# Performance work log

Measured on AMD Instinct MI355X. Metric: run time of the kernel, lower is better.

The kernel has to match this reference:

```python
import jax, jax.numpy as jnp
import numpy as np
from jax.scipy.linalg import solve_triangular

H, VD, M = 16, 64, 128
RIDGE = 0.01


def setup_inputs() -> dict:
    key = jax.random.key(0)
    ks = jax.random.split(key, 9)
    B, L, HD = 4, 2048, 1024
    s = 1.0 / np.sqrt(HD).astype(np.float32)
    return {
        "x": jax.random.normal(ks[0], (B, L, HD), dtype=jnp.float32),
        "cur_k": jnp.zeros((1,), dtype=jnp.float32),
        "input_mask": jnp.ones((B, L), dtype=jnp.float32),
        "Wq": jax.random.normal(ks[1], (HD, HD), dtype=jnp.float32) * s,
        "Wk": jax.random.normal(ks[2], (HD, HD), dtype=jnp.float32) * s,
        "Wv": jax.random.normal(ks[3], (HD, HD), dtype=jnp.float32) * s,
        "Wo": jax.random.normal(ks[4], (HD, HD), dtype=jnp.float32) * s,
        "bo": jax.random.normal(ks[5], (HD,), dtype=jnp.float32) * s,
        "rff_W": jax.random.normal(ks[6], (H, VD, M), dtype=jnp.float32),  # / lengthscale=1.0
        "rff_b": 2.0 * np.pi * jax.random.uniform(ks[7], (H, M), dtype=jnp.float32),
    }


def reference(x, cur_k, input_mask, Wq, Wk, Wv, Wo, bo, rff_W, rff_b):
    B, L, HD = x.shape
    scale = jnp.asarray(1.0 / np.sqrt(M), dtype=x.dtype)
    M2 = 2 * M

    def heads(t):  # [B,L,HD] -> [B,H,L,VD]
        return t.reshape(B, L, H, VD).transpose(0, 2, 1, 3)

    q = heads(x @ Wq.T)
    k = heads(x @ Wk.T)
    v = heads(x @ Wv.T)

    mask = input_mask[:, :L].astype(x.dtype)
    qmask = mask[:, None, :, None]  # [B,1,L,1]

    def rff(X):  # [B,H,L,VD] -> [B,H,L,2M]
        proj = jnp.einsum('bhld,hdm->bhlm', X, rff_W) + rff_b[None, :, None, :]
        return scale * jnp.concatenate([jnp.cos(proj), jnp.sin(proj)], axis=-1)

    PhiQ = rff(q)
    PhiK_w = rff(k) * qmask
    V_w = v * qmask

    G = jnp.einsum('bhlm,bhln->bhmn', PhiK_w, PhiK_w)  # [B,H,2M,2M]
    G = G + RIDGE * jnp.eye(M2, dtype=x.dtype)
    T = jnp.einsum('bhlm,bhld->bhmd', PhiK_w, V_w)      # [B,H,2M,VD]

    Lch = jnp.linalg.cholesky(G)
    y = solve_triangular(Lch, T, lower=True)
    W = solve_triangular(jnp.swapaxes(Lch, -2, -1), y, lower=False)

    out = jnp.einsum('bhlm,bhmd->bhld', PhiQ, W)        # [B,H,L,VD]
    # unsqueeze sample dim, permute to [B,1,L,H,VD], flatten heads -> [B,1,L,HD]
    samples = jnp.transpose(out, (0, 2, 1, 3)).reshape(B, L, HD)[:, None]
    samples = samples @ Wo.T + bo                        # W_O (dropout: eval no-op)
    samples = samples * qmask                            # [B,1,L,1] broadcast
    return samples
```

## Files before the change

kernel.cpp:

```cpp
#include <hip/hip_runtime.h>
#include <math.h>

#define B_ 4
#define L_ 2048
#define HD_ 1024
#define H_ 16
#define VD_ 64
#define M_ 128
#define M2_ 256
#define RIDGE_ 0.01f
#define SCALE_ 0.08838834764831845f

typedef unsigned short u16;
typedef __attribute__((ext_vector_type(8))) short short8;
typedef __attribute__((ext_vector_type(4))) float floatx4;

__device__ __forceinline__ u16 f2bf(float x) {
  unsigned u = __float_as_uint(x);
  unsigned r = u + 0x7fff + ((u >> 16) & 1);
  return (u16)(r >> 16);
}
__device__ __forceinline__ float bf2f(u16 h) {
  return __uint_as_float(((unsigned)h) << 16);
}
__device__ __forceinline__ void gload_lds16(const u16* g, u16* l) {
  __builtin_amdgcn_global_load_lds(
      (const __attribute__((address_space(1))) unsigned int*)g,
      (__attribute__((address_space(3))) unsigned int*)l, 16, 0, 0);
}
__device__ __forceinline__ void split4(float4 f, ushort4* h, float4* r) {
  h->x = f2bf(f.x); h->y = f2bf(f.y); h->z = f2bf(f.z); h->w = f2bf(f.w);
  r->x = f.x - bf2f(h->x); r->y = f.y - bf2f(h->y);
  r->z = f.z - bf2f(h->z); r->w = f.w - bf2f(h->w);
}

__global__ __launch_bounds__(256) void cvt_split_kernel(
    const float* __restrict__ src, u16* __restrict__ hi, u16* __restrict__ lo, int n4)
{
  int i = blockIdx.x * 256 + threadIdx.x;
  if (i < n4) {
    float4 f = ((const float4*)src)[i];
    ushort4 hv; float4 r;
    split4(f, &hv, &r);
    ushort4 lv = {f2bf(r.x), f2bf(r.y), f2bf(r.z), f2bf(r.w)};
    ((ushort4*)hi)[i] = hv;
    ((ushort4*)lo)[i] = lv;
  }
}

__global__ __launch_bounds__(256) void mfma_nt(
    const u16* __restrict__ A0, const u16* __restrict__ B0,
    float* __restrict__ C, int Ndim, int Kdim, int ldA, int ldB,
    const float* __restrict__ bias, const float* __restrict__ mask)
{
  __shared__ __align__(16) u16 a_sm[4096];
  __shared__ __align__(16) u16 b_sm[4096];
  const int tid = threadIdx.x;
  const int wave = tid >> 6, lane = tid & 63;
  const int m0 = blockIdx.y * 128, n0 = blockIdx.x * 128;
  const int wrow = (wave >> 1) * 64, wcol = (wave & 1) * 64;
  const int fm = lane & 15, q = lane >> 4;

  floatx4 acc[4][4];
#pragma unroll
  for (int i = 0; i < 4; ++i)
#pragma unroll
    for (int j = 0; j < 4; ++j) acc[i][j] = (floatx4){0.f, 0.f, 0.f, 0.f};

  const u16* Ag0 = A0 + (long)(m0 + lane) * ldA + wave * 8;
  const u16* Ag1 = A0 + (long)(m0 + 64 + lane) * ldA + wave * 8;
  const u16* Bg0 = B0 + (long)(n0 + lane) * ldB + wave * 8;
  const u16* Bg1 = B0 + (long)(n0 + 64 + lane) * ldB + wave * 8;
  u16* la0 = &a_sm[(wave * 128 + 0) * 8];
  u16* la1 = &a_sm[(wave * 128 + 64) * 8];
  u16* lb0 = &b_sm[(wave * 128 + 0) * 8];
  u16* lb1 = &b_sm[(wave * 128 + 64) * 8];

  for (int k0 = 0; k0 < Kdim; k0 += 32) {
    __syncthreads();
    gload_lds16(Ag0 + k0, la0);
    gload_lds16(Ag1 + k0, la1);
    gload_lds16(Bg0 + k0, lb0);
    gload_lds16(Bg1 + k0, lb1);
    __syncthreads();
    short8 af[4], bf[4];
#pragma unroll
    for (int i = 0; i < 4; ++i)
      af[i] = *(const short8*)&a_sm[(q * 128 + wrow + i * 16 + fm) * 8];
#pragma unroll
    for (int j = 0; j < 4; ++j)
      bf[j] = *(const short8*)&b_sm[(q * 128 + wcol + j * 16 + fm) * 8];
#pragma unroll
    for (int i = 0; i < 4; ++i)
#pragma unroll
      for (int j = 0; j < 4; ++j)
        acc[i][j] = __builtin_amdgcn_mfma_f32_16x16x32_bf16(af[i], bf[j], acc[i][j], 0, 0, 0);
  }

  const int colb = n0 + wcol + fm;
  const int rbase = m0 + wrow + (lane >> 4) * 4;
#pragma unroll
  for (int j = 0; j < 4; ++j) {
    int cg = colb + j * 16;
    float bb = bias ? bias[cg] : 0.f;
#pragma unroll
    for (int i = 0; i < 4; ++i) {
#pragma unroll
      for (int r = 0; r < 4; ++r) {
        int row = rbase + i * 16 + r;
        float val = acc[i][j][r];
        if (bias) val = (val + bb) * mask[row];
        C[(long)row * Ndim + cg] = val;
      }
    }
  }
}

__global__ __launch_bounds__(256) void mfma_qk3(
    const u16* __restrict__ Ah, const u16* __restrict__ Al,
    const u16* __restrict__ Bh, const u16* __restrict__ Bl,
    float* __restrict__ Cq, float* __restrict__ Ck)
{
  __shared__ __align__(16) u16 ah_sm[4096], al_sm[4096];
  __shared__ __align__(16) u16 bh_sm[4096], bl_sm[4096];
  const int tid = threadIdx.x;
  const int wave = tid >> 6, lane = tid & 63;
  const int m0 = blockIdx.y * 128, n0 = blockIdx.x * 128;
  const int wrow = (wave >> 1) * 64, wcol = (wave & 1) * 64;
  const int fm = lane & 15, q = lane >> 4;

  floatx4 acc[4][4];
#pragma unroll
  for (int i = 0; i < 4; ++i)
#pragma unroll
    for (int j = 0; j < 4; ++j) acc[i][j] = (floatx4){0.f, 0.f, 0.f, 0.f};

  const long a0o = (long)(m0 + lane) * 1024 + wave * 8;
  const long a1o = (long)(m0 + 64 + lane) * 1024 + wave * 8;
  const long b0o = (long)(n0 + lane) * 1024 + wave * 8;
  const long b1o = (long)(n0 + 64 + lane) * 1024 + wave * 8;
  u16* lah0 = &ah_sm[(wave * 128 + 0) * 8];
  u16* lah1 = &ah_sm[(wave * 128 + 64) * 8];
  u16* lal0 = &al_sm[(wave * 128 + 0) * 8];
  u16* lal1 = &al_sm[(wave * 128 + 64) * 8];
  u16* lbh0 = &bh_sm[(wave * 128 + 0) * 8];
  u16* lbh1 = &bh_sm[(wave * 128 + 64) * 8];
  u16* lbl0 = &bl_sm[(wave * 128 + 0) * 8];
  u16* lbl1 = &bl_sm[(wave * 128 + 64) * 8];

  for (int k0 = 0; k0 < 1024; k0 += 32) {
    __syncthreads();
    gload_lds16(Ah + a0o + k0, lah0);
    gload_lds16(Ah + a1o + k0, lah1);
    gload_lds16(Al + a0o + k0, lal0);
    gload_lds16(Al + a1o + k0, lal1);
    gload_lds16(Bh + b0o + k0, lbh0);
    gload_lds16(Bh + b1o + k0, lbh1);
    gload_lds16(Bl + b0o + k0, lbl0);
    gload_lds16(Bl + b1o + k0, lbl1);
    __syncthreads();
    short8 afh[4], afl[4], bfh[4], bfl[4];
#pragma unroll
    for (int i = 0; i < 4; ++i) {
      afh[i] = *(const short8*)&ah_sm[(q * 128 + wrow + i * 16 + fm) * 8];
      afl[i] = *(const short8*)&al_sm[(q * 128 + wrow + i * 16 + fm) * 8];
    }
#pragma unroll
    for (int j = 0; j < 4; ++j) {
      bfh[j] = *(const short8*)&bh_sm[(q * 128 + wcol + j * 16 + fm) * 8];
      bfl[j] = *(const short8*)&bl_sm[(q * 128 + wcol + j * 16 + fm) * 8];
    }
#pragma unroll
    for (int i = 0; i < 4; ++i)
#pragma unroll
      for (int j = 0; j < 4; ++j) {
        acc[i][j] = __builtin_amdgcn_mfma_f32_16x16x32_bf16(afh[i], bfh[j], acc[i][j], 0, 0, 0);
        acc[i][j] = __builtin_amdgcn_mfma_f32_16x16x32_bf16(afl[i], bfh[j], acc[i][j], 0, 0, 0);
        acc[i][j] = __builtin_amdgcn_mfma_f32_16x16x32_bf16(afh[i], bfl[j], acc[i][j], 0, 0, 0);
      }
  }

  float* Cp; int cb;
  if (n0 < 1024) { Cp = Cq; cb = n0; }
  else           { Cp = Ck; cb = n0 - 1024; }
  const int colb = cb + wcol + fm;
  const int rbase = m0 + wrow + (lane >> 4) * 4;
#pragma unroll
  for (int j = 0; j < 4; ++j) {
    int cg = colb + j * 16;
#pragma unroll
    for (int i = 0; i < 4; ++i)
#pragma unroll
      for (int r = 0; r < 4; ++r)
        Cp[(long)(rbase + i * 16 + r) * 1024 + cg] = acc[i][j][r];
  }
}

__global__ __launch_bounds__(256) void rff_k_t(
    const float* __restrict__ src, const float* __restrict__ mask,
    const float* __restrict__ rffW, const float* __restrict__ rffb,
    u16* __restrict__ pkh, u16* __restrict__ pkl, int b0)
{
  __shared__ __align__(16) float w_lds[64][132];
  __shared__ __align__(16) float x_lds[64][68];
  __shared__ float b_lds[128];
  const int l0 = blockIdx.x * 64;
  const int h = blockIdx.y, b = b0 + blockIdx.z;
  const int zloc = blockIdx.z * 16 + h;
  const int tid = threadIdx.x;

  const float* wsrc = rffW + h * 8192;
  for (int f = tid * 4; f < 8192; f += 1024) {
    int d = f >> 7, m = f & 127;
    *(float4*)&w_lds[d][m] = *(const float4*)&wsrc[f];
  }
  if (tid < 128) b_lds[tid] = rffb[h * 128 + tid];
  {
    int r = tid >> 2, c0 = (tid & 3) * 16;
    const float* srow = src + (long)(b * L_ + l0 + r) * 1024 + h * VD_ + c0;
    *(float4*)&x_lds[r][c0 + 0]  = *(const float4*)(srow + 0);
    *(float4*)&x_lds[r][c0 + 4]  = *(const float4*)(srow + 4);
    *(float4*)&x_lds[r][c0 + 8]  = *(const float4*)(srow + 8);
    *(float4*)&x_lds[r][c0 + 12] = *(const float4*)(srow + 12);
  }
  __syncthreads();

  const int ty = tid >> 4, tx = tid & 15;
  float acc[4][8];
  {
    float4 bb0 = *(const float4*)&b_lds[4 * tx];
    float4 bb1 = *(const float4*)&b_lds[4 * tx + 64];
#pragma unroll
    for (int i = 0; i < 4; ++i) {
      acc[i][0] = bb0.x; acc[i][1] = bb0.y; acc[i][2] = bb0.z; acc[i][3] = bb0.w;
      acc[i][4] = bb1.x; acc[i][5] = bb1.y; acc[i][6] = bb1.z; acc[i][7] = bb1.w;
    }
  }
#pragma unroll 8
  for (int kk = 0; kk < 64; ++kk) {
    float4 w0 = *(const float4*)&w_lds[kk][4 * tx];
    float4 w1 = *(const float4*)&w_lds[kk][4 * tx + 64];
    float xv[4];
#pragma unroll
    for (int i = 0; i < 4; ++i) xv[i] = x_lds[4 * ty + i][kk];
#pragma unroll
    for (int i = 0; i < 4; ++i) {
      acc[i][0] = fmaf(xv[i], w0.x, acc[i][0]);
      acc[i][1] = fmaf(xv[i], w0.y, acc[i][1]);
      acc[i][2] = fmaf(xv[i], w0.z, acc[i][2]);
      acc[i][3] = fmaf(xv[i], w0.w, acc[i][3]);
      acc[i][4] = fmaf(xv[i], w1.x, acc[i][4]);
      acc[i][5] = fmaf(xv[i], w1.y, acc[i][5]);
      acc[i][6] = fmaf(xv[i], w1.z, acc[i][6]);
      acc[i][7] = fmaf(xv[i], w1.w, acc[i][7]);
    }
  }
  float fi[4];
#pragma unroll
  for (int i = 0; i < 4; ++i) fi[i] = SCALE_ * mask[b * L_ + l0 + 4 * ty + i];
  float cvv[4][8], svv[4][8];
#pragma unroll
  for (int i = 0; i < 4; ++i)
#pragma unroll
    for (int jj = 0; jj < 8; ++jj) {
      float sv, cv;
      sincosf(acc[i][jj], &sv, &cv);
      cvv[i][jj] = cv * fi[i];
      svv[i][jj] = sv * fi[i];
    }
  const long lbase = l0 + 4 * ty;
  const long zbase = (long)zloc * 655360;
#pragma unroll
  for (int jj = 0; jj < 8; ++jj) {
    int mcol = (jj < 4) ? (4 * tx + jj) : (64 + 4 * tx + (jj - 4));
    ushort4 h4, l4;
    h4.x = f2bf(cvv[0][jj]); l4.x = f2bf(cvv[0][jj] - bf2f(h4.x));
    h4.y = f2bf(cvv[1][jj]); l4.y = f2bf(cvv[1][jj] - bf2f(h4.y));
    h4.z = f2bf(cvv[2][jj]); l4.z = f2bf(cvv[2][jj] - bf2f(h4.z));
    h4.w = f2bf(cvv[3][jj]); l4.w = f2bf(cvv[3][jj] - bf2f(h4.w));
    long base = zbase + (long)mcol * 2048 + lbase;
    *(ushort4*)&pkh[base] = h4;
    *(ushort4*)&pkl[base] = l4;
    ushort4 hs, ls;
    hs.x = f2bf(svv[0][jj]); ls.x = f2bf(svv[0][jj] - bf2f(hs.x));
    hs.y = f2bf(svv[1][jj]); ls.y = f2bf(svv[1][jj] - bf2f(hs.y));
    hs.z = f2bf(svv[2][jj]); ls.z = f2bf(svv[2][jj] - bf2f(hs.z));
    hs.w = f2bf(svv[3][jj]); ls.w = f2bf(svv[3][jj] - bf2f(hs.w));
    long base2 = zbase + (long)(mcol + 128) * 2048 + lbase;
    *(ushort4*)&pkh[base2] = hs;
    *(ushort4*)&pkl[base2] = ls;
  }
}

__global__ __launch_bounds__(256) void vt_kernel(
    const float* __restrict__ v, const float* __restrict__ mask,
    u16* __restrict__ pkh, u16* __restrict__ pkl, int b0)
{
  __shared__ float t[128][65];
  const int z = blockIdx.y;
  const int b = b0 + (z >> 4), h = z & 15;
  const int l0 = blockIdx.x * 128;
  const int tid = threadIdx.x;
  const int d = tid & 63, lg = tid >> 6;
  for (int i = 0; i < 128; i += 4) {
    int ll = i + lg;
    float mv = mask[b * L_ + l0 + ll];
    t[ll][d] = v[(long)(b * L_ + l0 + ll) * 1024 + h * 64 + d] * mv;
  }
  __syncthreads();
  const int d2 = tid >> 2, lofs = (tid & 3) * 32;
  long base = (long)z * 655360 + (long)(256 + d2) * 2048 + l0 + lofs;
  for (int j = 0; j < 32; j += 4) {
    float f0 = t[lofs + j + 0][d2], f1 = t[lofs + j + 1][d2];
    float f2 = t[lofs + j + 2][d2], f3 = t[lofs + j + 3][d2];
    ushort4 hv, lv;
    hv.x = f2bf(f0); lv.x = f2bf(f0 - bf2f(hv.x));
    hv.y = f2bf(f1); lv.y = f2bf(f1 - bf2f(hv.y));
    hv.z = f2bf(f2); lv.z = f2bf(f2 - bf2f(hv.z));
    hv.w = f2bf(f3); lv.w = f2bf(f3 - bf2f(hv.w));
    *(ushort4*)&pkh[base + j] = hv;
    *(ushort4*)&pkl[base + j] = lv;
  }
}

__global__ __launch_bounds__(256) void mfma_gt(
    const u16* __restrict__ pkh, const u16* __restrict__ pkl,
    float* __restrict__ Gp, float* __restrict__ Tp, int bh0)
{
  __shared__ __align__(16) u16 ah_sm[4096], al_sm[4096];
  __shared__ __align__(16) u16 bh_sm[2048], bl_sm[2048];
  const int tid = threadIdx.x;
  const int wave = tid >> 6, lane = tid & 63;
  const int z = blockIdx.z;
  const int mt = blockIdx.y & 1, kc = blockIdx.y >> 1;
  const int m0 = mt * 128, n0 = blockIdx.x * 64;
  const int wrow = (wave >> 1) * 64, wcol = (wave & 1) * 32;
  const int fm = lane & 15, q = lane >> 4;
  const long batch = (long)z * 655360;
  const u16* Ah = pkh + batch;
  const u16* Al = pkl + batch;

  floatx4 acc[4][2];
#pragma unroll
  for (int i = 0; i < 4; ++i)
#pragma unroll
    for (int j = 0; j < 2; ++j) acc[i][j] = (floatx4){0.f, 0.f, 0.f, 0.f};

  const long a0o = (long)(m0 + lane) * 2048 + wave * 8;
  const long a1o = (long)(m0 + 64 + lane) * 2048 + wave * 8;
  const long b0o = (long)(n0 + lane) * 2048 + wave * 8;
  u16* lah0 = &ah_sm[(wave * 128 + 0) * 8];
  u16* lah1 = &ah_sm[(wave * 128 + 64) * 8];
  u16* lal0 = &al_sm[(wave * 128 + 0) * 8];
  u16* lal1 = &al_sm[(wave * 128 + 64) * 8];
  u16* lbh = &bh_sm[(wave * 64) * 8];
  u16* lbl = &bl_sm[(wave * 64) * 8];

  const int kbeg = kc * 1024, kend = kbeg + 1024;
  for (int k0 = kbeg; k0 < kend; k0 += 32) {
    __syncthreads();
    gload_lds16(Ah + a0o + k0, lah0);
    gload_lds16(Ah + a1o + k0, lah1);
    gload_lds16(Al + a0o + k0, lal0);
    gload_lds16(Al + a1o + k0, lal1);
    gload_lds16(Ah + b0o + k0, lbh);
    gload_lds16(Al + b0o + k0, lbl);
    __syncthreads();
    short8 afh[4], afl[4], bfh[2], bfl[2];
#pragma unroll
    for (int i = 0; i < 4; ++i) {
      afh[i] = *(const short8*)&ah_sm[(q * 128 + wrow + i * 16 + fm) * 8];
      afl[i] = *(const short8*)&al_sm[(q * 128 + wrow + i * 16 + fm) * 8];
    }
#pragma unroll
    for (int j = 0; j < 2; ++j) {
      bfh[j] = *(const short8*)&bh_sm[(q * 64 + wcol + j * 16 + fm) * 8];
      bfl[j] = *(const short8*)&bl_sm[(q * 64 + wcol + j * 16 + fm) * 8];
    }
#pragma unroll
    for (int i = 0; i < 4; ++i)
#pragma unroll
      for (int j = 0; j < 2; ++j) {
        acc[i][j] = __builtin_amdgcn_mfma_f32_16x16x32_bf16(afh[i], bfh[j], acc[i][j], 0, 0, 0);
        acc[i][j] = __builtin_amdgcn_mfma_f32_16x16x32_bf16(afl[i], bfh[j], acc[i][j], 0, 0, 0);
        acc[i][j] = __builtin_amdgcn_mfma_f32_16x16x32_bf16(afh[i], bfl[j], acc[i][j], 0, 0, 0);
      }
  }

  const int bh = bh0 + z;
  float* Gb = Gp + (long)kc * 4194304;
  float* Tb = Tp + (long)kc * 1048576;
  const int rbase = m0 + wrow + (lane >> 4) * 4;
#pragma unroll
  for (int j = 0; j < 2; ++j) {
    int col = n0 + wcol + j * 16 + fm;
#pragma unroll
    for (int i = 0; i < 4; ++i)
#pragma unroll
      for (int r = 0; r < 4; ++r) {
        int row = rbase + i * 16 + r;
        float val = acc[i][j][r];
        if (n0 < 256) Gb[(long)bh * 65536 + (long)row * 256 + col] = val;
        else Tb[(long)bh * 16384 + (long)row * 64 + (col - 256)] = val;
      }
  }
}

__global__ __launch_bounds__(256) void reduce_gt_kernel(
    const float* __restrict__ Gp, float* __restrict__ G,
    const float* __restrict__ Tp, float* __restrict__ T)
{
  long i = (long)blockIdx.x * 256 + threadIdx.x;
  if (i < 1048576) {
    float4 a = ((const float4*)Gp)[i];
    float4 b = ((const float4*)(Gp + 4194304))[i];
    float4 o = {a.x + b.x, a.y + b.y, a.z + b.z, a.w + b.w};
    ((float4*)G)[i] = o;
  } else {
    long j = i - 1048576;
    float4 a = ((const float4*)Tp)[j];
    float4 b = ((const float4*)(Tp + 1048576))[j];
    float4 o = {a.x + b.x, a.y + b.y, a.z + b.z, a.w + b.w};
    ((float4*)T)[j] = o;
  }
}

__global__ __launch_bounds__(256) void mfma_out_k(
    const u16* __restrict__ ph, const u16* __restrict__ pl,
    const u16* __restrict__ wth, const u16* __restrict__ wtl,
    u16* __restrict__ oh)
{
  __shared__ __align__(16) u16 ah_sm[4096], al_sm[4096];
  __shared__ __align__(16) u16 bh_sm[2048], bl_sm[2048];
  const int tid = threadIdx.x;
  const int wave = tid >> 6, lane = tid & 63;
  const int bh = blockIdx.y;
  const int b = bh >> 4, h = bh & 15;
  const int l0 = blockIdx.x * 128;
  const int wrow = (wave >> 1) * 64, wcol = (wave & 1) * 32;
  const int fm = lane & 15, q = lane >> 4;
  const u16* Ah = ph + (long)bh * 524288 + (long)l0 * 256;
  const u16* Al = pl + (long)bh * 524288 + (long)l0 * 256;
  const u16* Bh = wth + (long)bh * 16384;
  const u16* Bl = wtl + (long)bh * 16384;

  floatx4 acc[4][2];
#pragma unroll
  for (int i = 0; i < 4; ++i)
#pragma unroll
    for (int j = 0; j < 2; ++j) acc[i][j] = (floatx4){0.f, 0.f, 0.f, 0.f};

  const long a0o = (long)lane * 256 + wave * 8;
  const long a1o = (long)(64 + lane) * 256 + wave * 8;
  const long b0o = (long)lane * 256 + wave * 8;
  u16* lah0 = &ah_sm[(wave * 128 + 0) * 8];
  u16* lah1 = &ah_sm[(wave * 128 + 64) * 8];
  u16* lal0 = &al_sm[(wave * 128 + 0) * 8];
  u16* lal1 = &al_sm[(wave * 128 + 64) * 8];
  u16* lbh = &bh_sm[(wave * 64) * 8];
  u16* lbl = &bl_sm[(wave * 64) * 8];

  for (int k0 = 0; k0 < 256; k0 += 32) {
    __syncthreads();
    gload_lds16(Ah + a0o + k0, lah0);
    gload_lds16(Ah + a1o + k0, lah1);
    gload_lds16(Al + a0o + k0, lal0);
    gload_lds16(Al + a1o + k0, lal1);
    gload_lds16(Bh + b0o + k0, lbh);
    gload_lds16(Bl + b0o + k0, lbl);
    __syncthreads();
    short8 afh[4], afl[4], bfh[2], bfl[2];
#pragma unroll
    for (int i = 0; i < 4; ++i) {
      afh[i] = *(const short8*)&ah_sm[(q * 128 + wrow + i * 16 + fm) * 8];
      afl[i] = *(const short8*)&al_sm[(q * 128 + wrow + i * 16 + fm) * 8];
    }
#pragma unroll
    for (int j = 0; j < 2; ++j) {
      bfh[j] = *(const short8*)&bh_sm[(q * 64 + wcol + j * 16 + fm) * 8];
      bfl[j] = *(const short8*)&bl_sm[(q * 64 + wcol + j * 16 + fm) * 8];
    }
#pragma unroll
    for (int i = 0; i < 4; ++i)
#pragma unroll
      for (int j = 0; j < 2; ++j) {
        acc[i][j] = __builtin_amdgcn_mfma_f32_16x16x32_bf16(afh[i], bfh[j], acc[i][j], 0, 0, 0);
        acc[i][j] = __builtin_amdgcn_mfma_f32_16x16x32_bf16(afl[i], bfh[j], acc[i][j], 0, 0, 0);
        acc[i][j] = __builtin_amdgcn_mfma_f32_16x16x32_bf16(afh[i], bfl[j], acc[i][j], 0, 0, 0);
      }
  }

  const int rbase = l0 + wrow + (lane >> 4) * 4;
#pragma unroll
  for (int j = 0; j < 2; ++j) {
    int col = h * 64 + wcol + j * 16 + fm;
#pragma unroll
    for (int i = 0; i < 4; ++i)
#pragma unroll
      for (int r = 0; r < 4; ++r)
        oh[(long)(b * L_ + rbase + i * 16 + r) * 1024 + col] = f2bf(acc[i][j][r]);
  }
}

__global__ __launch_bounds__(512) void chol_rffq_wo_kernel(
    float* __restrict__ Gw,
    const float* __restrict__ qsrc,
    const float* __restrict__ rffW, const float* __restrict__ rffb,
    u16* __restrict__ ph, u16* __restrict__ pl,
    const float* __restrict__ Wo, u16* __restrict__ wo_hi)
{
  extern __shared__ float sm[];
  const int bx = blockIdx.x;
  const int tid = threadIdx.x;

  if (bx < 64) {
    float* panel = sm;
    float* invD  = sm + 4352;
    float* Gb = Gw + (long)bx * 65536;

    for (int p = 0; p < 16; ++p) {
      if (tid < 64) {
        const int i = tid & 15;
        float r[16];
#pragma unroll
        for (int k = 0; k < 16; ++k) r[k] = Gb[(16 * p + i) * 256 + 16 * p + k];
        r[i] += RIDGE_;
#pragma unroll
        for (int j = 0; j < 16; ++j) {
          float dj = __shfl(r[j], j);
          float dinv = 1.0f / sqrtf(dj);
          r[j] *= dinv;
          float Lij = r[j];
#pragma unroll
          for (int k = j + 1; k < 16; ++k) {
            float Lkj = __shfl(r[j], k);
            r[k] = fmaf(-Lij, Lkj, r[k]);
          }
        }
        float x[16];
#pragma unroll
        for (int j = 0; j < 16; ++j) {
          float s = (i == j) ? 1.0f : 0.0f;
#pragma unroll
          for (int k = 0; k < j; ++k) {
            float Ljk = __shfl(r[k], j);
            s = fmaf(-Ljk, x[k], s);
          }
          float Ljj = __shfl(r[j], j);
          x[j] = s / Ljj;
        }
        if (tid < 16) {
#pragma unroll
          for (int j = 0; j < 16; ++j) {
            invD[j * 17 + tid] = x[j];
            Gb[(16 * p + j) * 256 + 16 * p + tid] = x[j];
          }
        }
      }
      __syncthreads();

      const int nIb = 15 - p;
      if (nIb == 0) break;
      const int nrows = nIb * 16;
      const int r0 = 16 * (p + 1);

      for (int f = tid; f < nrows * 16; f += 512) {
        int rr = f >> 4, cc = f & 15;
        panel[(r0 + rr) * 17 + cc] = Gb[(long)(r0 + rr) * 256 + 16 * p + cc];
      }
      __syncthreads();

      float outv[8];
#pragma unroll
      for (int s = 0; s < 8; ++s) {
        int f = tid + s * 512;
        if (f < nrows * 16) {
          int rr = f >> 4, j = f & 15;
          const float* arow = &panel[(r0 + rr) * 17];
          const float* dcol = &invD[j * 17];
          float s2 = 0.f;
#pragma unroll
          for (int k = 0; k < 16; ++k) s2 = fmaf(arow[k], dcol[k], s2);
          outv[s] = s2;
        }
      }
      __syncthreads();
#pragma unroll
      for (int s = 0; s < 8; ++s) {
        int f = tid + s * 512;
        if (f < nrows * 16) {
          int rr = f >> 4, j = f & 15;
          panel[(r0 + rr) * 17 + j] = outv[s];
          Gb[(long)(r0 + rr) * 256 + 16 * p + j] = outv[s];
        }
      }
      __syncthreads();

      const int npairs = nIb * (nIb + 1) / 2;
      const int g = tid >> 4, t = tid & 15;
      const int tx = t & 3, ty = t >> 2;
      for (int pi0 = 0; pi0 < npairs; pi0 += 32) {
        int pi = pi0 + g;
        if (pi < npairs) {
          int a = 0; while ((a + 1) * (a + 2) / 2 <= pi) ++a;
          int b2 = pi - a * (a + 1) / 2;
          int I = p + 1 + a, J = p + 1 + b2;
          float c4[4][4];
#pragma unroll
          for (int ii = 0; ii < 4; ++ii) {
            float4 cv = *(const float4*)&Gb[(long)(16 * I + 4 * ty + ii) * 256 + 16 * J + 4 * tx];
            c4[ii][0] = cv.x; c4[ii][1] = cv.y; c4[ii][2] = cv.z; c4[ii][3] = cv.w;
          }
#pragma unroll
          for (int kk = 0; kk < 16; ++kk) {
            float av[4], bv[4];
#pragma unroll
            for (int ii = 0; ii < 4; ++ii) av[ii] = panel[(16 * I + 4 * ty + ii) * 17 + kk];
#pragma unroll
            for (int jj = 0; jj < 4; ++jj) bv[jj] = panel[(16 * J + 4 * tx + jj) * 17 + kk];
#pragma unroll
            for (int ii = 0; ii < 4; ++ii)
#pragma unroll
              for (int jj = 0; jj < 4; ++jj)
                c4[ii][jj] = fmaf(-av[ii], bv[jj], c4[ii][jj]);
          }
#pragma unroll
          for (int ii = 0; ii < 4; ++ii) {
            float4 cv = {c4[ii][0], c4[ii][1], c4[ii][2], c4[ii][3]};
            *(float4*)&Gb[(long)(16 * I + 4 * ty + ii) * 256 + 16 * J + 4 * tx] = cv;
          }
        }
      }
      __syncthreads();
    }
  } else if (bx < 64 + 2048) {
    const int id = bx - 64;
    const int l0 = (id & 31) * 64;
    const int h = (id >> 5) & 15;
    const int b = id >> 9;
    float* w_lds = sm;
    float* x_lds = sm + 8448;
    float* b_lds = sm + 12800;

    const float* wsrc = rffW + h * 8192;
    for (int f = tid * 4; f < 8192; f += 2048) {
      int d = f >> 7, m = f & 127;
      *(float4*)&w_lds[d * 132 + m] = *(const float4*)&wsrc[f];
    }
    if (tid < 128) b_lds[tid] = rffb[h * 128 + tid];
    {
      int r = tid >> 3, c0 = (tid & 7) * 8;
      const float* srow = qsrc + (long)(b * L_ + l0 + r) * 1024 + h * VD_ + c0;
      *(float4*)&x_lds[r * 68 + c0 + 0] = *(const float4*)(srow + 0);
      *(float4*)&x_lds[r * 68 + c0 + 4] = *(const float4*)(srow + 4);
    }
    __syncthreads();

    const int sub = tid >> 8;
    const int t = tid & 255;
    const int ty = t >> 4, tx = t & 15;
    const int rrow = sub * 32 + 2 * ty;
    float acc[2][8];
    {
      float4 bb0 = *(const float4*)&b_lds[4 * tx];
      float4 bb1 = *(const float4*)&b_lds[4 * tx + 64];
#pragma unroll
      for (int i = 0; i < 2; ++i) {
        acc[i][0] = bb0.x; acc[i][1] = bb0.y; acc[i][2] = bb0.z; acc[i][3] = bb0.w;
        acc[i][4] = bb1.x; acc[i][5] = bb1.y; acc[i][6] = bb1.z; acc[i][7] = bb1.w;
      }
    }
#pragma unroll 8
    for (int kk = 0; kk < 64; ++kk) {
      float4 w0 = *(const float4*)&w_lds[kk * 132 + 4 * tx];
      float4 w1 = *(const float4*)&w_lds[kk * 132 + 4 * tx + 64];
      float xv[2];
#pragma unroll
      for (int i = 0; i < 2; ++i) xv[i] = x_lds[(rrow + i) * 68 + kk];
#pragma unroll
      for (int i = 0; i < 2; ++i) {
        acc[i][0] = fmaf(xv[i], w0.x, acc[i][0]);
        acc[i][1] = fmaf(xv[i], w0.y, acc[i][1]);
        acc[i][2] = fmaf(xv[i], w0.z, acc[i][2]);
        acc[i][3] = fmaf(xv[i], w0.w, acc[i][3]);
        acc[i][4] = fmaf(xv[i], w1.x, acc[i][4]);
        acc[i][5] = fmaf(xv[i], w1.y, acc[i][5]);
        acc[i][6] = fmaf(xv[i], w1.z, acc[i][6]);
        acc[i][7] = fmaf(xv[i], w1.w, acc[i][7]);
      }
    }
#pragma unroll
    for (int i = 0; i < 2; ++i) {
      int l = l0 + rrow + i;
      float4 c0, c1, s0, s1;
      float sv, cv;
      sincosf(acc[i][0], &sv, &cv); c0.x = cv * SCALE_; s0.x = sv * SCALE_;
      sincosf(acc[i][1], &sv, &cv); c0.y = cv * SCALE_; s0.y = sv * SCALE_;
      sincosf(acc[i][2], &sv, &cv); c0.z = cv * SCALE_; s0.z = sv * SCALE_;
      sincosf(acc[i][3], &sv, &cv); c0.w = cv * SCALE_; s0.w = sv * SCALE_;
      sincosf(acc[i][4], &sv, &cv); c1.x = cv * SCALE_; s1.x = sv * SCALE_;
      sincosf(acc[i][5], &sv, &cv); c1.y = cv * SCALE_; s1.y = sv * SCALE_;
      sincosf(acc[i][6], &sv, &cv); c1.z = cv * SCALE_; s1.z = sv * SCALE_;
      sincosf(acc[i][7], &sv, &cv); c1.w = cv * SCALE_; s1.w = sv * SCALE_;
      long base = ((long)(b * H_ + h) * L_ + l) * M2_;
      ushort4 hv; float4 r4;
      split4(c0, &hv, &r4);
      *(ushort4*)&ph[base + 4 * tx] = hv;
      *(ushort4*)&pl[base + 4 * tx] = (ushort4){f2bf(r4.x), f2bf(r4.y), f2bf(r4.z), f2bf(r4.w)};
      split4(c1, &hv, &r4);
      *(ushort4*)&ph[base + 64 + 4 * tx] = hv;
      *(ushort4*)&pl[base + 64 + 4 * tx] = (ushort4){f2bf(r4.x), f2bf(r4.y), f2bf(r4.z), f2bf(r4.w)};
      split4(s0, &hv, &r4);
      *(ushort4*)&ph[base + 128 + 4 * tx] = hv;
      *(ushort4*)&pl[base + 128 + 4 * tx] = (ushort4){f2bf(r4.x), f2bf(r4.y), f2bf(r4.z), f2bf(r4.w)};
      split4(s1, &hv, &r4);
      *(ushort4*)&ph[base + 192 + 4 * tx] = hv;
      *(ushort4*)&pl[base + 192 + 4 * tx] = (ushort4){f2bf(r4.x), f2bf(r4.y), f2bf(r4.z), f2bf(r4.w)};
    }
  } else {
    const int id2 = bx - (64 + 2048);
    int idx = id2 * 512 + tid;
    for (int i = idx; i < 262144; i += 65536) {
      float4 f = ((const float4*)Wo)[i];
      ushort4 hv = {f2bf(f.x), f2bf(f.y), f2bf(f.z), f2bf(f.w)};
      ((ushort4*)wo_hi)[i] = hv;
    }
  }
}

__global__ __launch_bounds__(256) void tri_solve_kernel(
    const float* __restrict__ Gw, const float* __restrict__ T,
    u16* __restrict__ wth, u16* __restrict__ wtl)
{
  __shared__ float Y[256 * 17];
  __shared__ float tmp[16 * 17];
  const int bh = blockIdx.y;
  const int d0 = blockIdx.x * 16;
  const int tid = threadIdx.x;
  const int i = tid >> 4, d = tid & 15;
  const float* Gb = Gw + (long)bh * 65536;
  const float* Tb = T + (long)bh * 16384;

  for (int r = i; r < 256; r += 16) Y[r * 17 + d] = Tb[r * 64 + d0 + d];
  __syncthreads();

  for (int J = 0; J < 16; ++J) {
    float acc = Y[(J * 16 + i) * 17 + d];
    for (int c = 0; c < J; ++c) {
      const float* Lblk = &Gb[(long)(16 * J + i) * 256 + 16 * c];
#pragma unroll
      for (int k = 0; k < 16; k += 4) {
        float4 l4 = *(const float4*)&Lblk[k];
        acc = fmaf(-l4.x, Y[(c * 16 + k + 0) * 17 + d], acc);
        acc = fmaf(-l4.y, Y[(c * 16 + k + 1) * 17 + d], acc);
        acc = fmaf(-l4.z, Y[(c * 16 + k + 2) * 17 + d], acc);
        acc = fmaf(-l4.w, Y[(c * 16 + k + 3) * 17 + d], acc);
      }
    }
    tmp[i * 17 + d] = acc;
    __syncthreads();
    const float* invD = &Gb[(long)(16 * J + i) * 256 + 16 * J];
    float y = 0.f;
#pragma unroll
    for (int k = 0; k < 16; ++k) y = fmaf(invD[k], tmp[k * 17 + d], y);
    Y[(J * 16 + i) * 17 + d] = y;
    __syncthreads();
  }

  for (int J = 15; J >= 0; --J) {
    float acc = Y[(J * 16 + i) * 17 + d];
    for (int I = J + 1; I < 16; ++I) {
#pragma unroll
      for (int k = 0; k < 16; ++k)
        acc = fmaf(-Gb[(long)(16 * I + k) * 256 + 16 * J + i], Y[(I * 16 + k) * 17 + d], acc);
    }
    tmp[i * 17 + d] = acc;
    __syncthreads();
    float w = 0.f;
#pragma unroll
    for (int k = 0; k < 16; ++k)
      w = fmaf(Gb[(long)(16 * J + k) * 256 + 16 * J + i], tmp[k * 17 + d], w);
    Y[(J * 16 + i) * 17 + d] = w;
    __syncthreads();
  }

  for (int f = tid; f < 16 * 256; f += 256) {
    int dc = f >> 8, m = f & 255;
    float val = Y[m * 17 + dc];
    u16 h = f2bf(val);
    long o = (long)bh * 16384 + (long)(d0 + dc) * 256 + m;
    wth[o] = h;
    wtl[o] = f2bf(val - bf2f(h));
  }
}

__global__ void ws_too_small_kernel(float* out) { out[0] = 12345.0f; }

extern "C" void kernel_launch(void* const* d_in, const int* in_sizes, int n_in,
                              void* d_out, int out_size, void* d_ws, size_t ws_size,
                              hipStream_t stream) {
  const float* x    = (const float*)d_in[0];
  const float* mask = (const float*)d_in[2];
  const float* Wq   = (const float*)d_in[3];
  const float* Wk   = (const float*)d_in[4];
  const float* Wv   = (const float*)d_in[5];
  const float* Wo   = (const float*)d_in[6];
  const float* bo   = (const float*)d_in[7];
  const float* rffW = (const float*)d_in[8];
  const float* rffb = (const float*)d_in[9];
  float* out = (float*)d_out;
  float* ws  = (float*)d_ws;

  const size_t needed = 58720256UL * 4UL;
  if (ws_size < needed) {
    ws_too_small_kernel<<<1, 1, 0, stream>>>(out);
    return;
  }
  float* q = ws;
  u16* oh_bf = (u16*)ws;
  float* kbuf = ws + 8388608;
  float* T    = ws + 8388608;
  float* G    = ws + 9437184;
  u16* big16 = (u16*)(ws + 16777216);
  u16* x_hi = big16;
  u16* x_lo = big16 + 8388608;
  u16* w_hi = big16 + 16777216;
  u16* w_lo = big16 + 19922944;
  u16* pk_hi = big16;
  u16* pk_lo = big16 + 20971520;
  float* Gp = ws + 37748736;
  float* Tp = ws + 46137344;
  u16* phiq_hi = big16;
  u16* phiq_lo = big16 + 33554432;
  float* v = ws + 50331648;
  u16* wt_hi = (u16*)(ws + 50331648);
  u16* wt_lo = wt_hi + 1048576;
  u16* wo_hi = wt_hi + 2097152;

  hipFuncSetAttribute((const void*)chol_rffq_wo_kernel,
                      hipFuncAttributeMaxDynamicSharedMemorySize, 51712);

  dim3 blk(256);

  cvt_split_kernel<<<8192, blk, 0, stream>>>(x, x_hi, x_lo, 2097152);
  cvt_split_kernel<<<1024, blk, 0, stream>>>(Wq, w_hi,           w_lo,           262144);
  cvt_split_kernel<<<1024, blk, 0, stream>>>(Wk, w_hi + 1048576, w_lo + 1048576, 262144);
  cvt_split_kernel<<<1024, blk, 0, stream>>>(Wv, w_hi + 2097152, w_lo + 2097152, 262144);

  mfma_qk3<<<dim3(16, 64), blk, 0, stream>>>(x_hi, x_lo, w_hi, w_lo, q, kbuf);
  mfma_nt<<<dim3(8, 64), blk, 0, stream>>>(x_hi, w_hi + 2097152, v,
                                           1024, 1024, 1024, 1024, nullptr, nullptr);

  for (int half = 0; half < 2; ++half) {
    int b0 = half * 2, bh0 = half * 32;
    rff_k_t<<<dim3(32, 16, 2), blk, 0, stream>>>(kbuf, mask, rffW, rffb, pk_hi, pk_lo, b0);
    vt_kernel<<<dim3(16, 32), blk, 0, stream>>>(v, mask, pk_hi, pk_lo, b0);
    mfma_gt<<<dim3(5, 4, 32), blk, 0, stream>>>(pk_hi, pk_lo, Gp, Tp, bh0);
  }

  reduce_gt_kernel<<<5120, blk, 0, stream>>>(Gp, G, Tp, T);

  chol_rffq_wo_kernel<<<dim3(64 + 2048 + 128), dim3(512), 51712, stream>>>(
      G, q, rffW, rffb, phiq_hi, phiq_lo, Wo, wo_hi);

  tri_solve_kernel<<<dim3(4, 64), dim3(256), 0, stream>>>(G, T, wt_hi, wt_lo);

  mfma_out_k<<<dim3(16, 64), blk, 0, stream>>>(phiq_hi, phiq_lo, wt_hi, wt_lo, oh_bf);

  mfma_nt<<<dim3(8, 64), blk, 0, stream>>>(oh_bf, wo_hi, out, 1024, 1024, 1024, 1024, bo, mask);
}
```

Baseline: 895.5 us.

## Double-buffer LDS tiles in all MFMA GEMM kernels to overlap loads with compute

Each of the four MFMA GEMM kernels now keeps two LDS buffers. The next K-slice is loaded into one buffer while the current slice is read and multiplied from the other, which halves the number of barriers per K-step. The aim is to hide global-to-LDS latency behind MFMA work. The cost is twice the LDS footprint (up to 64KB in the qk3 kernel), which may reduce occupancy. Correctness also depends on the async LDS loads being complete at the barrier.

```diff
diff --git a/kernel.cpp b/kernel.cpp
--- a/kernel.cpp
+++ b/kernel.cpp
@@ -53,13 +53,14 @@
     float* __restrict__ C, int Ndim, int Kdim, int ldA, int ldB,
     const float* __restrict__ bias, const float* __restrict__ mask)
 {
-  __shared__ __align__(16) u16 a_sm[4096];
-  __shared__ __align__(16) u16 b_sm[4096];
+  __shared__ __align__(16) u16 a_sm[2][4096];
+  __shared__ __align__(16) u16 b_sm[2][4096];
   const int tid = threadIdx.x;
   const int wave = tid >> 6, lane = tid & 63;
   const int m0 = blockIdx.y * 128, n0 = blockIdx.x * 128;
   const int wrow = (wave >> 1) * 64, wcol = (wave & 1) * 64;
   const int fm = lane & 15, q = lane >> 4;
+  const int lofs = wave * 1024;
 
   floatx4 acc[4][4];
 #pragma unroll
@@ -71,30 +72,37 @@
   const u16* Ag1 = A0 + (long)(m0 + 64 + lane) * ldA + wave * 8;
   const u16* Bg0 = B0 + (long)(n0 + lane) * ldB + wave * 8;
   const u16* Bg1 = B0 + (long)(n0 + 64 + lane) * ldB + wave * 8;
-  u16* la0 = &a_sm[(wave * 128 + 0) * 8];
-  u16* la1 = &a_sm[(wave * 128 + 64) * 8];
-  u16* lb0 = &b_sm[(wave * 128 + 0) * 8];
-  u16* lb1 = &b_sm[(wave * 128 + 64) * 8];
-
-  for (int k0 = 0; k0 < Kdim; k0 += 32) {
-    __syncthreads();
-    gload_lds16(Ag0 + k0, la0);
-    gload_lds16(Ag1 + k0, la1);
-    gload_lds16(Bg0 + k0, lb0);
-    gload_lds16(Bg1 + k0, lb1);
-    __syncthreads();
-    short8 af[4], bf[4];
+
+  auto stage = [&](int d, int k0) {
+    gload_lds16(Ag0 + k0, &a_sm[d][lofs]);
+    gload_lds16(Ag1 + k0, &a_sm[d][lofs + 512]);
+    gload_lds16(Bg0 + k0, &b_sm[d][lofs]);
+    gload_lds16(Bg1 + k0, &b_sm[d][lofs + 512]);
+  };
+  auto compute = [&](int d) {
+    short8 af[4], bfv[4];
 #pragma unroll
     for (int i = 0; i < 4; ++i)
-      af[i] = *(const short8*)&a_sm[(q * 128 + wrow + i * 16 + fm) * 8];
+      af[i] = *(const short8*)&a_sm[d][(q * 128 + wrow + i * 16 + fm) * 8];
 #pragma unroll
     for (int j = 0; j < 4; ++j)
-      bf[j] = *(const short8*)&b_sm[(q * 128 + wcol + j * 16 + fm) * 8];
+      bfv[j] = *(const short8*)&b_sm[d][(q * 128 + wcol + j * 16 + fm) * 8];
 #pragma unroll
     for (int i = 0; i < 4; ++i)
 #pragma unroll
       for (int j = 0; j < 4; ++j)
-        acc[i][j] = __builtin_amdgcn_mfma_f32_16x16x32_bf16(af[i], bf[j], acc[i][j], 0, 0, 0);
+        acc[i][j] = __builtin_amdgcn_mfma_f32_16x16x32_bf16(af[i], bfv[j], acc[i][j], 0, 0, 0);
+  };
+
+  stage(0, 0);
+  __syncthreads();
+  for (int k0 = 0; k0 < Kdim; k0 += 64) {
+    if (k0 + 32 < Kdim) stage(1, k0 + 32);
+    compute(0);
+    __syncthreads();
+    if (k0 + 64 < Kdim) stage(0, k0 + 64);
+    compute(1);
+    __syncthreads();
   }
 
   const int colb = n0 + wcol + fm;
@@ -121,13 +129,14 @@
     const u16* __restrict__ Bh, const u16* __restrict__ Bl,
     float* __restrict__ Cq, float* __restrict__ Ck)
 {
-  __shared__ __align__(16) u16 ah_sm[4096], al_sm[4096];
-  __shared__ __align__(16) u16 bh_sm[4096], bl_sm[4096];
+  __shared__ __align__(16) u16 ah_sm[2][4096], al_sm[2][4096];
+  __shared__ __align__(16) u16 bh_sm[2][4096], bl_sm[2][4096];
   const int tid = threadIdx.x;
   const int wave = tid >> 6, lane = tid & 63;
   const int m0 = blockIdx.y * 128, n0 = blockIdx.x * 128;
   const int wrow = (wave >> 1) * 64, wcol = (wave & 1) * 64;
   const int fm = lane & 15, q = lane >> 4;
+  const int lofs = wave * 1024;
 
   floatx4 acc[4][4];
 #pragma unroll
@@ -139,36 +148,28 @@
   const long a1o = (long)(m0 + 64 + lane) * 1024 + wave * 8;
   const long b0o = (long)(n0 + lane) * 1024 + wave * 8;
   const long b1o = (long)(n0 + 64 + lane) * 1024 + wave * 8;
-  u16* lah0 = &ah_sm[(wave * 128 + 0) * 8];
-  u16* lah1 = &ah_sm[(wave * 128 + 64) * 8];
-  u16* lal0 = &al_sm[(wave * 128 + 0) * 8];
-  u16* lal1 = &al_sm[(wave * 128 + 64) * 8];
-  u16* lbh0 = &bh_sm[(wave * 128 + 0) * 8];
-  u16* lbh1 = &bh_sm[(wave * 128 + 64) * 8];
-  u16* lbl0 = &bl_sm[(wave * 128 + 0) * 8];
-  u16* lbl1 = &bl_sm[(wave * 128 + 64) * 8];
-
-  for (int k0 = 0; k0 < 1024; k0 += 32) {
-    __syncthreads();
-    gload_lds16(Ah + a0o + k0, lah0);
-    gload_lds16(Ah + a1o + k0, lah1);
-    gload_lds16(Al + a0o + k0, lal0);
-    gload_lds16(Al + a1o + k0, lal1);
-    gload_lds16(Bh + b0o + k0, lbh0);
-    gload_lds16(Bh + b1o + k0, lbh1);
-    gload_lds16(Bl + b0o + k0, lbl0);
-    gload_lds16(Bl + b1o + k0, lbl1);
-    __syncthreads();
+
+  auto stage = [&](int d, int k0) {
+    gload_lds16(Ah + a0o + k0, &ah_sm[d][lofs]);
+    gload_lds16(Ah + a1o + k0, &ah_sm[d][lofs + 512]);
+    gload_lds16(Al + a0o + k0, &al_sm[d][lofs]);
+    gload_lds16(Al + a1o + k0, &al_sm[d][lofs + 512]);
+    gload_lds16(Bh + b0o + k0, &bh_sm[d][lofs]);
+    gload_lds16(Bh + b1o + k0, &bh_sm[d][lofs + 512]);
+    gload_lds16(Bl + b0o + k0, &bl_sm[d][lofs]);
+    gload_lds16(Bl + b1o + k0, &bl_sm[d][lofs + 512]);
+  };
+  auto compute = [&](int d) {
     short8 afh[4], afl[4], bfh[4], bfl[4];
 #pragma unroll
     for (int i = 0; i < 4; ++i) {
-      afh[i] = *(const short8*)&ah_sm[(q * 128 + wrow + i * 16 + fm) * 8];
-      afl[i] = *(const short8*)&al_sm[(q * 128 + wrow + i * 16 + fm) * 8];
+      afh[i] = *(const short8*)&ah_sm[d][(q * 128 + wrow + i * 16 + fm) * 8];
+      afl[i] = *(const short8*)&al_sm[d][(q * 128 + wrow + i * 16 + fm) * 8];
     }
 #pragma unroll
     for (int j = 0; j < 4; ++j) {
-      bfh[j] = *(const short8*)&bh_sm[(q * 128 + wcol + j * 16 + fm) * 8];
-      bfl[j] = *(const short8*)&bl_sm[(q * 128 + wcol + j * 16 + fm) * 8];
+      bfh[j] = *(const short8*)&bh_sm[d][(q * 128 + wcol + j * 16 + fm) * 8];
+      bfl[j] = *(const short8*)&bl_sm[d][(q * 128 + wcol + j * 16 + fm) * 8];
     }
 #pragma unroll
     for (int i = 0; i < 4; ++i)
@@ -178,6 +179,17 @@
         acc[i][j] = __builtin_amdgcn_mfma_f32_16x16x32_bf16(afl[i], bfh[j], acc[i][j], 0, 0, 0);
         acc[i][j] = __builtin_amdgcn_mfma_f32_16x16x32_bf16(afh[i], bfl[j], acc[i][j], 0, 0, 0);
       }
+  };
+
+  stage(0, 0);
+  __syncthreads();
+  for (int k0 = 0; k0 < 1024; k0 += 64) {
+    if (k0 + 32 < 1024) stage(1, k0 + 32);
+    compute(0);
+    __syncthreads();
+    if (k0 + 64 < 1024) stage(0, k0 + 64);
+    compute(1);
+    __syncthreads();
   }
 
   float* Cp; int cb;
@@ -327,8 +339,8 @@
     const u16* __restrict__ pkh, const u16* __restrict__ pkl,
     float* __restrict__ Gp, float* __restrict__ Tp, int bh0)
 {
-  __shared__ __align__(16) u16 ah_sm[4096], al_sm[4096];
-  __shared__ __align__(16) u16 bh_sm[2048], bl_sm[2048];
+  __shared__ __align__(16) u16 ah_sm[2][4096], al_sm[2][4096];
+  __shared__ __align__(16) u16 bh_sm[2][2048], bl_sm[2][2048];
   const int tid = threadIdx.x;
   const int wave = tid >> 6, lane = tid & 63;
   const int z = blockIdx.z;
@@ -339,6 +351,8 @@
   const long batch = (long)z * 655360;
   const u16* Ah = pkh + batch;
   const u16* Al = pkl + batch;
+  const int lofsA = wave * 1024;
+  const int lofsB = wave * 512;
 
   floatx4 acc[4][2];
 #pragma unroll
@@ -349,33 +363,26 @@
   const long a0o = (long)(m0 + lane) * 2048 + wave * 8;
   const long a1o = (long)(m0 + 64 + lane) * 2048 + wave * 8;
   const long b0o = (long)(n0 + lane) * 2048 + wave * 8;
-  u16* lah0 = &ah_sm[(wave * 128 + 0) * 8];
-  u16* lah1 = &ah_sm[(wave * 128 + 64) * 8];
-  u16* lal0 = &al_sm[(wave * 128 + 0) * 8];
-  u16* lal1 = &al_sm[(wave * 128 + 64) * 8];
-  u16* lbh = &bh_sm[(wave * 64) * 8];
-  u16* lbl = &bl_sm[(wave * 64) * 8];
-
-  const int kbeg = kc * 1024, kend = kbeg + 1024;
-  for (int k0 = kbeg; k0 < kend; k0 += 32) {
-    __syncthreads();
-    gload_lds16(Ah + a0o + k0, lah0);
-    gload_lds16(Ah + a1o + k0, lah1);
-    gload_lds16(Al + a0o + k0, lal0);
-    gload_lds16(Al + a1o + k0, lal1);
-    gload_lds16(Ah + b0o + k0, lbh);
-    gload_lds16(Al + b0o + k0, lbl);
-    __syncthreads();
+
+  auto stage = [&](int d, int k0) {
+    gload_lds16(Ah + a0o + k0, &ah_sm[d][lofsA]);
+    gload_lds16(Ah + a1o + k0, &ah_sm[d][lofsA + 512]);
+    gload_lds16(Al + a0o + k0, &al_sm[d][lofsA]);
+    gload_lds16(Al + a1o + k0, &al_sm[d][lofsA + 512]);
+    gload_lds16(Ah + b0o + k0, &bh_sm[d][lofsB]);
+    gload_lds16(Al + b0o + k0, &bl_sm[d][lofsB]);
+  };
+  auto compute = [&](int d) {
     short8 afh[4], afl[4], bfh[2], bfl[2];
 #pragma unroll
     for (int i = 0; i < 4; ++i) {
-      afh[i] = *(const short8*)&ah_sm[(q * 128 + wrow + i * 16 + fm) * 8];
-      afl[i] = *(const short8*)&al_sm[(q * 128 + wrow + i * 16 + fm) * 8];
+      afh[i] = *(const short8*)&ah_sm[d][(q * 128 + wrow + i * 16 + fm) * 8];
+      afl[i] = *(const short8*)&al_sm[d][(q * 128 + wrow + i * 16 + fm) * 8];
     }
 #pragma unroll
     for (int j = 0; j < 2; ++j) {
-      bfh[j] = *(const short8*)&bh_sm[(q * 64 + wcol + j * 16 + fm) * 8];
-      bfl[j] = *(const short8*)&bl_sm[(q * 64 + wcol + j * 16 + fm) * 8];
+      bfh[j] = *(const short8*)&bh_sm[d][(q * 64 + wcol + j * 16 + fm) * 8];
+      bfl[j] = *(const short8*)&bl_sm[d][(q * 64 + wcol + j * 16 + fm) * 8];
     }
 #pragma unroll
     for (int i = 0; i < 4; ++i)
@@ -385,6 +392,18 @@
         acc[i][j] = __builtin_amdgcn_mfma_f32_16x16x32_bf16(afl[i], bfh[j], acc[i][j], 0, 0, 0);
         acc[i][j] = __builtin_amdgcn_mfma_f32_16x16x32_bf16(afh[i], bfl[j], acc[i][j], 0, 0, 0);
       }
+  };
+
+  const int kbeg = kc * 1024, kend = kbeg + 1024;
+  stage(0, kbeg);
+  __syncthreads();
+  for (int k0 = kbeg; k0 < kend; k0 += 64) {
+    if (k0 + 32 < kend) stage(1, k0 + 32);
+    compute(0);
+    __syncthreads();
+    if (k0 + 64 < kend) stage(0, k0 + 64);
+    compute(1);
+    __syncthreads();
   }
 
   const int bh = bh0 + z;
@@ -430,8 +449,8 @@
     const u16* __restrict__ wth, const u16* __restrict__ wtl,
     u16* __restrict__ oh)
 {
-  __shared__ __align__(16) u16 ah_sm[4096], al_sm[4096];
-  __shared__ __align__(16) u16 bh_sm[2048], bl_sm[2048];
+  __shared__ __align__(16) u16 ah_sm[2][4096], al_sm[2][4096];
+  __shared__ __align__(16) u16 bh_sm[2][2048], bl_sm[2][2048];
   const int tid = threadIdx.x;
   const int wave = tid >> 6, lane = tid & 63;
   const int bh = blockIdx.y;
@@ -443,6 +462,8 @@
   const u16* Al = pl + (long)bh * 524288 + (long)l0 * 256;
   const u16* Bh = wth + (long)bh * 16384;
   const u16* Bl = wtl + (long)bh * 16384;
+  const int lofsA = wave * 1024;
+  const int lofsB = wave * 512;
 
   floatx4 acc[4][2];
 #pragma unroll
@@ -453,32 +474,26 @@
   const long a0o = (long)lane * 256 + wave * 8;
   const long a1o = (long)(64 + lane) * 256 + wave * 8;
   const long b0o = (long)lane * 256 + wave * 8;
-  u16* lah0 = &ah_sm[(wave * 128 + 0) * 8];
-  u16* lah1 = &ah_sm[(wave * 128 + 64) * 8];
-  u16* lal0 = &al_sm[(wave * 128 + 0) * 8];
-  u16* lal1 = &al_sm[(wave * 128 + 64) * 8];
-  u16* lbh = &bh_sm[(wave * 64) * 8];
-  u16* lbl = &bl_sm[(wave * 64) * 8];
-
-  for (int k0 = 0; k0 < 256; k0 += 32) {
-    __syncthreads();
-    gload_lds16(Ah + a0o + k0, lah0);
-    gload_lds16(Ah + a1o + k0, lah1);
-    gload_lds16(Al + a0o + k0, lal0);
-    gload_lds16(Al + a1o + k0, lal1);
-    gload_lds16(Bh + b0o + k0, lbh);
-    gload_lds16(Bl + b0o + k0, lbl);
-    __syncthreads();
+
+  auto stage = [&](int d, int k0) {
+    gload_lds16(Ah + a0o + k0, &ah_sm[d][lofsA]);
+    gload_lds16(Ah + a1o + k0, &ah_sm[d][lofsA + 512]);
+    gload_lds16(Al + a0o + k0, &al_sm[d][lofsA]);
+    gload_lds16(Al + a1o + k0, &al_sm[d][lofsA + 512]);
+    gload_lds16(Bh + b0o + k0, &bh_sm[d][lofsB]);
+    gload_lds16(Bl + b0o + k0, &bl_sm[d][lofsB]);
+  };
+  auto compute = [&](int d) {
     short8 afh[4], afl[4], bfh[2], bfl[2];
 #pragma unroll
     for (int i = 0; i < 4; ++i) {
-      afh[i] = *(const short8*)&ah_sm[(q * 128 + wrow + i * 16 + fm) * 8];
-      afl[i] = *(const short8*)&al_sm[(q * 128 + wrow + i * 16 + fm) * 8];
+      afh[i] = *(const short8*)&ah_sm[d][(q * 128 + wrow + i * 16 + fm) * 8];
+      afl[i] = *(const short8*)&al_sm[d][(q * 128 + wrow + i * 16 + fm) * 8];
     }
 #pragma unroll
     for (int j = 0; j < 2; ++j) {
-      bfh[j] = *(const short8*)&bh_sm[(q * 64 + wcol + j * 16 + fm) * 8];
-      bfl[j] = *(const short8*)&bl_sm[(q * 64 + wcol + j * 16 + fm) * 8];
+      bfh[j] = *(const short8*)&bh_sm[d][(q * 64 + wcol + j * 16 + fm) * 8];
+      bfl[j] = *(const short8*)&bl_sm[d][(q * 64 + wcol + j * 16 + fm) * 8];
     }
 #pragma unroll
     for (int i = 0; i < 4; ++i)
@@ -488,6 +503,17 @@
         acc[i][j] = __builtin_amdgcn_mfma_f32_16x16x32_bf16(afl[i], bfh[j], acc[i][j], 0, 0, 0);
         acc[i][j] = __builtin_amdgcn_mfma_f32_16x16x32_bf16(afh[i], bfl[j], acc[i][j], 0, 0, 0);
       }
+  };
+
+  stage(0, 0);
+  __syncthreads();
+  for (int k0 = 0; k0 < 256; k0 += 64) {
+    if (k0 + 32 < 256) stage(1, k0 + 32);
+    compute(0);
+    __syncthreads();
+    if (k0 + 64 < 256) stage(0, k0 + 64);
+    compute(1);
+    __syncthreads();
   }
 
   const int rbase = l0 + wrow + (lane >> 4) * 4;
```

New measurement: 911.0 us. No clear change (+1.7%).
